# Kernel tuning notes

Measured on AMD Instinct MI355X. Metric: run time of the kernel, lower is better.

## Reference

```python
import jax, jax.numpy as jnp
import numpy as np

N, E = 50000, 800000
S, V, RBF_DIM = 128, 16, 16
RBF_DMAX = 20.0
MSG_NORM = 10.0
EPS = 1e-8
DVH_M = V + 1            # message GVP: dim_vectors_in = V + 1 (edge direction appended), dim_h = max(17,16) = 17
FIN_M = S + RBF_DIM      # message GVP scalar input = node scalars + rbf(dist)
DVH_U = 2 * V            # update GVP: dim_vectors_in = 2V (node + aggregated), dim_h = 32
FIN_U = 2 * S


def _rbf(D):
    # [E] -> [E, RBF_DIM], matches torch _rbf with D_min=0, D_max=20, D_count=16
    D_mu = jnp.linspace(0.0, RBF_DMAX, RBF_DIM)
    D_sigma = RBF_DMAX / RBF_DIM
    return jnp.exp(-(((D[:, None] - D_mu[None, :]) / D_sigma) ** 2))


def _gvp(s, v, Wh, Wu, Wf, bf, Wg, bg):
    # s: [n, F_in], v: [n, V_in, 3]; faithful to GVP.forward with sigmoid vector gating
    Vh = jnp.einsum('nvc,vh->nhc', v, Wh)          # [n, H, 3]
    Vu = jnp.einsum('nhc,ho->noc', Vh, Wu)         # [n, V_out, 3]
    sh = jnp.sqrt(jnp.clip(jnp.sum(Vh * Vh, -1), EPS))  # _norm_no_nan
    feats_out = jax.nn.silu(jnp.concatenate([s, sh], -1) @ Wf + bf)
    gate = jax.nn.sigmoid(feats_out @ Wg + bg)[..., None]
    return feats_out, gate * Vu


def _gvp_layernorm(s, v, gamma, beta):
    mu = jnp.mean(s, -1, keepdims=True)
    var = jnp.mean((s - mu) ** 2, -1, keepdims=True)
    s_out = (s - mu) / jnp.sqrt(var + 1e-5) * gamma + beta
    vn = jnp.clip(jnp.sum(v * v, -1, keepdims=True), EPS)        # [N, V, 1]
    vn = jnp.sqrt(jnp.mean(vn, -2, keepdims=True) + 1e-5) + 1e-5  # [N, 1, 1]
    return s_out, v / vn


def setup_inputs() -> dict:
    key = jax.random.key(0)
    ks = jax.random.split(key, 14)
    rn = lambda k, shp, sc: (jax.random.normal(k, shp, dtype=jnp.float32) * sc)
    inp = {
        's': rn(ks[0], (N, S), 1.0),
        'v': rn(ks[1], (N, V, 3), 1.0),
        'x': rn(ks[2], (N, 3), 5.0),
        # message GVP params
        'Wh_m': rn(ks[3], (DVH_M, DVH_M), 1.0 / np.sqrt(DVH_M)),
        'Wu_m': rn(ks[4], (DVH_M, V), 1.0 / np.sqrt(DVH_M)),
        'Wf_m': rn(ks[5], (DVH_M + FIN_M, S), 1.0 / np.sqrt(DVH_M + FIN_M)),
        'bf_m': jnp.zeros((S,), jnp.float32),
        'Wg_m': rn(ks[6], (S, V), 1.0 / np.sqrt(S)),
        'bg_m': jnp.zeros((V,), jnp.float32),
        # update GVP params
        'Wh_u': rn(ks[7], (DVH_U, DVH_U), 1.0 / np.sqrt(DVH_U)),
        'Wu_u': rn(ks[8], (DVH_U, V), 1.0 / np.sqrt(DVH_U)),
        'Wf_u': rn(ks[9], (DVH_U + FIN_U, S), 1.0 / np.sqrt(DVH_U + FIN_U)),
        'bf_u': jnp.zeros((S,), jnp.float32),
        'Wg_u': rn(ks[10], (S, V), 1.0 / np.sqrt(S)),
        'bg_u': jnp.zeros((V,), jnp.float32),
        # layernorm
        'ln_g': jnp.ones((S,), jnp.float32),
        'ln_b': jnp.zeros((S,), jnp.float32),
        'edge_index': jax.random.randint(ks[11], (2, E), 0, N),
    }
    return inp


def reference(s, v, x, Wh_m, Wu_m, Wf_m, bf_m, Wg_m, bg_m,
              Wh_u, Wu_u, Wf_u, bf_u, Wg_u, bg_u, ln_g, ln_b, edge_index):
    src, dst = edge_index[0], edge_index[1]
    # gather + geometric edge features
    dx = x[dst] - x[src]                                   # [E, 3]
    dist = jnp.sqrt(jnp.clip(jnp.sum(dx * dx, -1), EPS))    # [E]
    unit = dx / dist[:, None]
    v_in = jnp.concatenate([v[src], unit[:, None, :]], 1)   # [E, V+1, 3]
    s_in = jnp.concatenate([s[src], _rbf(dist)], -1)        # [E, S+RBF]
    # message GVP
    ms, mv = _gvp(s_in, v_in, Wh_m, Wu_m, Wf_m, bf_m, Wg_m, bg_m)
    # scatter-reduce + message norm
    agg_s = jax.ops.segment_sum(ms, dst, num_segments=N) / MSG_NORM   # [N, S]
    agg_v = jax.ops.segment_sum(mv, dst, num_segments=N) / MSG_NORM   # [N, V, 3]
    # update GVP on concatenated node + aggregated messages
    us, uv = _gvp(jnp.concatenate([s, agg_s], -1), jnp.concatenate([v, agg_v], 1),
                  Wh_u, Wu_u, Wf_u, bf_u, Wg_u, bg_u)
    # residual + GVPLayerNorm
    return _gvp_layernorm(s + us, v + uv, ln_g, ln_b)
```

## Files before the change

### kernel.cpp

```cpp
#include <hip/hip_runtime.h>
#include <hip/hip_bf16.h>
#include <math.h>

#define N_NODES 50000
#define E_EDGES 800000
#define S_DIM 128
#define V_DIM 16
#define HM 17
#define KM 161
#define HU 32
#define KU 288

#define EB 32
#define LDA 164
#define NB 32
#define LDA2 292

__device__ __forceinline__ float bf2f(unsigned short u) {
    union { unsigned int i; float f; } w; w.i = ((unsigned int)u) << 16; return w.f;
}
__device__ __forceinline__ unsigned short f2bf(float f) {
    union { float f; unsigned int i; } w; w.f = f;
    unsigned int x = w.i;
    x += 0x7fff + ((x >> 16) & 1);
    return (unsigned short)(x >> 16);
}
__device__ __forceinline__ float silu_f(float x) { return x / (1.f + __expf(-x)); }
__device__ __forceinline__ float sigm_f(float x) { return 1.f / (1.f + __expf(-x)); }
__device__ __forceinline__ float ldf(const void* p, int i, int m) {
    if (m) return ((const float*)p)[i];
    return bf2f(((const unsigned short*)p)[i]);
}

__global__ void detect_kernel(const unsigned short* __restrict__ s_us,
                              int* __restrict__ flag) {
    int t = threadIdx.x;
    int huge = 0;
    for (int k = 0; k < 16; ++k) {
        unsigned short u = s_us[2 * (t + 64 * k)];
        int e = (u >> 7) & 0xFF;
        if (e > 140) huge = 1;
    }
    if (huge) atomicOr(flag, 1);
}

__global__ __launch_bounds__(256, 4) void edge_kernel(
    const void* sP, const void* vP, const void* xP,
    const void* WhP, const void* WuP, const void* WfP,
    const void* bfP, const void* WgP, const void* bgP,
    const int* __restrict__ ei,
    const int* __restrict__ flagp,
    float* __restrict__ agg_s,
    float* __restrict__ agg_v)
{
    __shared__ float A[EB * LDA];
    __shared__ float Bs[2048];
    __shared__ float WhWu[HM * 16];
    __shared__ float gates[EB * 16];
    __shared__ int srcb[EB], dstb[EB];

    const int t = threadIdx.x;
    const int e0 = blockIdx.x * EB;
    const int m = flagp[0];

    if (t < EB) {
        srcb[t] = ei[e0 + t];
        dstb[t] = ei[E_EDGES + e0 + t];
    }
    if (m) {
        const float* Wh = (const float*)WhP;
        const float* Wu = (const float*)WuP;
        for (int i = t; i < HM * HM; i += 256) gates[i] = Wh[i];
        for (int i = t; i < HM * 16; i += 256) Bs[1664 + i] = Wu[i];
    } else {
        const unsigned short* Wh = (const unsigned short*)WhP;
        const unsigned short* Wu = (const unsigned short*)WuP;
        for (int i = t; i < HM * HM; i += 256) gates[i] = bf2f(Wh[i]);
        for (int i = t; i < HM * 16; i += 256) Bs[1664 + i] = bf2f(Wu[i]);
    }
    __syncthreads();

    for (int idx = t; idx < HM * 16; idx += 256) {
        int vv = idx / 16, o = idx % 16;
        float acc = 0.f;
        for (int h = 0; h < HM; ++h)
            acc += gates[vv * HM + h] * Bs[1664 + h * 16 + o];
        WhWu[idx] = acc;
    }
    {
        int tj = t & 31, te = t >> 5;
        if (m) {
            const float* sF = (const float*)sP;
            for (int r = 0; r < 4; ++r) {
                int e = te + 8 * r;
                float4 u = *(const float4*)(sF + (size_t)srcb[e] * S_DIM + tj * 4);
                float* a = &A[e * LDA + tj * 4];
                a[0] = u.x; a[1] = u.y; a[2] = u.z; a[3] = u.w;
            }
        } else {
            const unsigned short* sU = (const unsigned short*)sP;
            for (int r = 0; r < 4; ++r) {
                int e = te + 8 * r;
                ushort4 u = *(const ushort4*)(sU + (size_t)srcb[e] * S_DIM + tj * 4);
                float* a = &A[e * LDA + tj * 4];
                a[0] = bf2f(u.x); a[1] = bf2f(u.y); a[2] = bf2f(u.z); a[3] = bf2f(u.w);
            }
        }
    }
    if (t < 128) {
        int e = t >> 2, q = t & 3;
        int src = srcb[e];
        float* vin = &Bs[e * 52 + q * 12];
        if (m) {
            const float* vp = (const float*)vP + (size_t)src * 48 + q * 12;
            for (int i = 0; i < 3; ++i) {
                float4 u = *(const float4*)(vp + i * 4);
                vin[i * 4 + 0] = u.x; vin[i * 4 + 1] = u.y;
                vin[i * 4 + 2] = u.z; vin[i * 4 + 3] = u.w;
            }
        } else {
            const unsigned short* vp = (const unsigned short*)vP + (size_t)src * 48 + q * 12;
            for (int i = 0; i < 3; ++i) {
                ushort4 u = *(const ushort4*)(vp + i * 4);
                vin[i * 4 + 0] = bf2f(u.x); vin[i * 4 + 1] = bf2f(u.y);
                vin[i * 4 + 2] = bf2f(u.z); vin[i * 4 + 3] = bf2f(u.w);
            }
        }
        if (q == 0) {
            int dst = dstb[e];
            float dxc[3]; float d2 = 0.f;
            for (int c = 0; c < 3; ++c) {
                float xs = ldf(xP, src * 3 + c, m);
                float xd = ldf(xP, dst * 3 + c, m);
                dxc[c] = xd - xs; d2 += dxc[c] * dxc[c];
            }
            float dist = sqrtf(fmaxf(d2, 1e-8f));
            float inv = 1.f / dist;
            for (int c = 0; c < 3; ++c) Bs[e * 52 + 48 + c] = dxc[c] * inv;
            for (int k = 0; k < 16; ++k) {
                float mu = (20.f / 15.f) * (float)k;
                float z = (dist - mu) * (1.f / 1.25f);
                A[e * LDA + 128 + k] = __expf(-z * z);
            }
        }
    }
    __syncthreads();

    for (int idx = t; idx < EB * HM; idx += 256) {
        int e = idx / HM, h = idx % HM;
        const float* vin = &Bs[e * 52];
        float vh0 = 0.f, vh1 = 0.f, vh2 = 0.f;
        for (int vv = 0; vv < HM; ++vv) {
            float w = gates[vv * HM + h];
            vh0 += vin[vv * 3 + 0] * w;
            vh1 += vin[vv * 3 + 1] * w;
            vh2 += vin[vv * 3 + 2] * w;
        }
        A[e * LDA + 144 + h] = sqrtf(fmaxf(vh0 * vh0 + vh1 * vh1 + vh2 * vh2, 1e-8f));
    }
    float vureg[6];
    for (int r = 0; r < 6; ++r) {
        int idx = t + 256 * r;
        int e = idx / 48, oc = idx % 48, o = oc / 3, c = oc % 3;
        const float* vin = &Bs[e * 52];
        float acc = 0.f;
        for (int vv = 0; vv < HM; ++vv)
            acc += vin[vv * 3 + c] * WhWu[vv * 16 + o];
        vureg[r] = acc;
    }
    __syncthreads();

    const int tj = t & 15, te = t >> 4;
    const int eb = te * 2;
    float acc[2][8];
    #pragma unroll
    for (int i = 0; i < 2; ++i)
        #pragma unroll
        for (int j = 0; j < 8; ++j) acc[i][j] = 0.f;

    for (int kk = 0; kk < KM; kk += 16) {
        int kmax = min(16, KM - kk);
        if (m) {
            const float* WfF = (const float*)WfP;
            for (int idx = t; idx < kmax * 32; idx += 256) {
                int kt = idx >> 5, col4 = (idx & 31) * 4;
                float4 u = *(const float4*)(WfF + (size_t)(kk + kt) * 128 + col4);
                float* b = &Bs[kt * 128 + col4];
                b[0] = u.x; b[1] = u.y; b[2] = u.z; b[3] = u.w;
            }
        } else {
            const unsigned short* WfU = (const unsigned short*)WfP;
            for (int idx = t; idx < kmax * 32; idx += 256) {
                int kt = idx >> 5, col4 = (idx & 31) * 4;
                ushort4 u = *(const ushort4*)(WfU + (size_t)(kk + kt) * 128 + col4);
                float* b = &Bs[kt * 128 + col4];
                b[0] = bf2f(u.x); b[1] = bf2f(u.y); b[2] = bf2f(u.z); b[3] = bf2f(u.w);
            }
        }
        __syncthreads();
        for (int kt = 0; kt < kmax; ++kt) {
            float a0 = A[(eb + 0) * LDA + kk + kt];
            float a1 = A[(eb + 1) * LDA + kk + kt];
            const float* brow = &Bs[kt * 128 + tj];
            #pragma unroll
            for (int jj = 0; jj < 8; ++jj) {
                float b = brow[16 * jj];
                acc[0][jj] += a0 * b; acc[1][jj] += a1 * b;
            }
        }
        __syncthreads();
    }
    float breg[8];
    #pragma unroll
    for (int jj = 0; jj < 8; ++jj) breg[jj] = ldf(bfP, tj + 16 * jj, m);
    #pragma unroll
    for (int i = 0; i < 2; ++i) {
        int e = eb + i;
        float* aout = &A[e * LDA];
        float* gp = &agg_s[(size_t)dstb[e] * S_DIM];
        #pragma unroll
        for (int jj = 0; jj < 8; ++jj) {
            int col = tj + 16 * jj;
            float f = silu_f(acc[i][jj] + breg[jj]);
            aout[col] = f;
            atomicAdd(&gp[col], f);
        }
    }
    __syncthreads();
    if (m) {
        const float* Wg = (const float*)WgP;
        for (int i = t; i < 2048; i += 256) Bs[i] = Wg[i];
    } else {
        const unsigned short* Wg = (const unsigned short*)WgP;
        for (int i = t; i < 2048; i += 256) Bs[i] = bf2f(Wg[i]);
    }
    __syncthreads();
    for (int r = 0; r < 2; ++r) {
        int idx = t + 256 * r;
        int e = idx / 16, o = idx % 16;
        const float* fe = &A[e * LDA];
        float g = ldf(bgP, o, m);
        for (int j = 0; j < S_DIM; ++j)
            g += fe[j] * Bs[j * 16 + o];
        gates[idx] = sigm_f(g);
    }
    __syncthreads();
    for (int r = 0; r < 6; ++r) {
        int idx = t + 256 * r;
        int e = idx / 48, oc = idx % 48, o = oc / 3;
        float mvv = vureg[r] * gates[e * 16 + o];
        atomicAdd(&agg_v[(size_t)dstb[e] * 48 + oc], mvv);
    }
}

__global__ __launch_bounds__(256) void node_kernel(
    const void* sP, const void* vP,
    const void* WhP, const void* WuP, const void* WfP,
    const void* bfP, const void* WgP, const void* bgP,
    const void* lngP, const void* lnbP,
    const int* __restrict__ flagp,
    const float* __restrict__ agg_s,
    const float* __restrict__ agg_v,
    void* outP)
{
    __shared__ float A2[NB * LDA2];
    __shared__ float Bs2[4096];
    __shared__ float WhWu2[HU * 16];
    __shared__ float gates2[NB * 16];
    __shared__ float WhS[HU * HU];
    __shared__ float mu_s[NB], rstd_s[NB], vn_s[NB];

    const int t = threadIdx.x;
    const int n0 = blockIdx.x * NB;
    const int m = flagp[0];

    if (m) {
        const float* Wh = (const float*)WhP;
        const float* Wu = (const float*)WuP;
        for (int i = t; i < HU * HU; i += 256) WhS[i] = Wh[i];
        for (int i = t; i < HU * 16; i += 256) gates2[i] = Wu[i];
    } else {
        const unsigned short* Wh = (const unsigned short*)WhP;
        const unsigned short* Wu = (const unsigned short*)WuP;
        for (int i = t; i < HU * HU; i += 256) WhS[i] = bf2f(Wh[i]);
        for (int i = t; i < HU * 16; i += 256) gates2[i] = bf2f(Wu[i]);
    }
    if (m) {
        const float* sF = (const float*)sP;
        for (int idx = t; idx < NB * 32; idx += 256) {
            int ni = idx >> 5, col4 = (idx & 31) * 4;
            int n = n0 + ni;
            float* a = &A2[ni * LDA2 + col4];
            if (n < N_NODES) {
                float4 u = *(const float4*)(sF + (size_t)n * 128 + col4);
                a[0] = u.x; a[1] = u.y; a[2] = u.z; a[3] = u.w;
            } else { a[0] = a[1] = a[2] = a[3] = 0.f; }
        }
    } else {
        const unsigned short* sU = (const unsigned short*)sP;
        for (int idx = t; idx < NB * 32; idx += 256) {
            int ni = idx >> 5, col4 = (idx & 31) * 4;
            int n = n0 + ni;
            float* a = &A2[ni * LDA2 + col4];
            if (n < N_NODES) {
                ushort4 u = *(const ushort4*)(sU + (size_t)n * 128 + col4);
                a[0] = bf2f(u.x); a[1] = bf2f(u.y); a[2] = bf2f(u.z); a[3] = bf2f(u.w);
            } else { a[0] = a[1] = a[2] = a[3] = 0.f; }
        }
    }
    for (int idx = t; idx < NB * 32; idx += 256) {
        int ni = idx >> 5, col4 = (idx & 31) * 4;
        int n = n0 + ni;
        float* a = &A2[ni * LDA2 + 128 + col4];
        if (n < N_NODES) {
            float4 u = *(const float4*)(agg_s + (size_t)n * 128 + col4);
            a[0] = u.x * 0.1f; a[1] = u.y * 0.1f; a[2] = u.z * 0.1f; a[3] = u.w * 0.1f;
        } else { a[0] = a[1] = a[2] = a[3] = 0.f; }
    }
    for (int idx = t; idx < NB * 96; idx += 256) {
        int ni = idx / 96, vc = idx % 96;
        int n = n0 + ni;
        float val = 0.f;
        if (n < N_NODES)
            val = (vc < 48) ? ldf(vP, n * 48 + vc, m)
                            : agg_v[(size_t)n * 48 + (vc - 48)] * 0.1f;
        Bs2[ni * 100 + vc] = val;
    }
    __syncthreads();
    for (int idx = t; idx < HU * 16; idx += 256) {
        int vv = idx / 16, o = idx % 16;
        float acc = 0.f;
        for (int h = 0; h < HU; ++h)
            acc += WhS[vv * HU + h] * gates2[h * 16 + o];
        WhWu2[idx] = acc;
    }
    for (int idx = t; idx < NB * HU; idx += 256) {
        int ni = idx / HU, h = idx % HU;
        const float* vc = &Bs2[ni * 100];
        float vh0 = 0.f, vh1 = 0.f, vh2 = 0.f;
        for (int vv = 0; vv < HU; ++vv) {
            float w = WhS[vv * HU + h];
            vh0 += vc[vv * 3 + 0] * w; vh1 += vc[vv * 3 + 1] * w; vh2 += vc[vv * 3 + 2] * w;
        }
        A2[ni * LDA2 + 256 + h] = sqrtf(fmaxf(vh0 * vh0 + vh1 * vh1 + vh2 * vh2, 1e-8f));
    }
    __syncthreads();
    float vureg[6];
    for (int r = 0; r < 6; ++r) {
        int idx = t + 256 * r;
        int ni = idx / 48, oc = idx % 48, o = oc / 3, c = oc % 3;
        const float* vc = &Bs2[ni * 100];
        float acc = 0.f;
        for (int vv = 0; vv < HU; ++vv)
            acc += vc[vv * 3 + c] * WhWu2[vv * 16 + o];
        vureg[r] = acc;
    }
    __syncthreads();

    const int tj = t & 15, tn = t >> 4;
    const int nb = tn * 2;
    float acc[2][8];
    #pragma unroll
    for (int i = 0; i < 2; ++i)
        #pragma unroll
        for (int j = 0; j < 8; ++j) acc[i][j] = 0.f;

    for (int kk = 0; kk < KU; kk += 32) {
        if (m) {
            const float* WfF = (const float*)WfP;
            for (int idx = t; idx < 32 * 32; idx += 256) {
                int kt = idx >> 5, col4 = (idx & 31) * 4;
                float4 u = *(const float4*)(WfF + (size_t)(kk + kt) * 128 + col4);
                float* b = &Bs2[kt * 128 + col4];
                b[0] = u.x; b[1] = u.y; b[2] = u.z; b[3] = u.w;
            }
        } else {
            const unsigned short* WfU = (const unsigned short*)WfP;
            for (int idx = t; idx < 32 * 32; idx += 256) {
                int kt = idx >> 5, col4 = (idx & 31) * 4;
                ushort4 u = *(const ushort4*)(WfU + (size_t)(kk + kt) * 128 + col4);
                float* b = &Bs2[kt * 128 + col4];
                b[0] = bf2f(u.x); b[1] = bf2f(u.y); b[2] = bf2f(u.z); b[3] = bf2f(u.w);
            }
        }
        __syncthreads();
        for (int kt = 0; kt < 32; ++kt) {
            float a0 = A2[(nb + 0) * LDA2 + kk + kt];
            float a1 = A2[(nb + 1) * LDA2 + kk + kt];
            const float* brow = &Bs2[kt * 128 + tj];
            #pragma unroll
            for (int jj = 0; jj < 8; ++jj) {
                float b = brow[16 * jj];
                acc[0][jj] += a0 * b; acc[1][jj] += a1 * b;
            }
        }
        __syncthreads();
    }
    float breg[8];
    #pragma unroll
    for (int jj = 0; jj < 8; ++jj) breg[jj] = ldf(bfP, tj + 16 * jj, m);
    #pragma unroll
    for (int i = 0; i < 2; ++i) {
        float* aout = &A2[(nb + i) * LDA2 + 128];
        #pragma unroll
        for (int jj = 0; jj < 8; ++jj)
            aout[tj + 16 * jj] = silu_f(acc[i][jj] + breg[jj]);
    }
    __syncthreads();
    if (m) {
        const float* Wg = (const float*)WgP;
        for (int i = t; i < 2048; i += 256) Bs2[i] = Wg[i];
    } else {
        const unsigned short* Wg = (const unsigned short*)WgP;
        for (int i = t; i < 2048; i += 256) Bs2[i] = bf2f(Wg[i]);
    }
    __syncthreads();
    for (int r = 0; r < 2; ++r) {
        int idx = t + 256 * r;
        int ni = idx / 16, o = idx % 16;
        const float* fe = &A2[ni * LDA2 + 128];
        float g = ldf(bgP, o, m);
        for (int j = 0; j < 128; ++j)
            g += fe[j] * Bs2[j * 16 + o];
        gates2[idx] = sigm_f(g);
    }
    __syncthreads();
    for (int r = 0; r < 6; ++r) {
        int idx = t + 256 * r;
        int ni = idx / 48, oc = idx % 48, o = oc / 3;
        int n = n0 + ni;
        float vres = 0.f;
        if (n < N_NODES)
            vres = ldf(vP, n * 48 + oc, m) + vureg[r] * gates2[ni * 16 + o];
        Bs2[ni * 48 + oc] = vres;
    }
    __syncthreads();
    if (t < NB) {
        const float* arow = &A2[t * LDA2];
        float sum = 0.f, sumsq = 0.f;
        for (int j = 0; j < 128; ++j) {
            float xr = arow[j] + arow[128 + j];
            sum += xr; sumsq += xr * xr;
        }
        float mu = sum * (1.f / 128.f);
        float var = sumsq * (1.f / 128.f) - mu * mu;
        mu_s[t] = mu;
        rstd_s[t] = rsqrtf(fmaxf(var, 0.f) + 1e-5f);
        const float* vr = &Bs2[t * 48];
        float accv = 0.f;
        for (int o = 0; o < 16; ++o) {
            float mm = vr[o*3]*vr[o*3] + vr[o*3+1]*vr[o*3+1] + vr[o*3+2]*vr[o*3+2];
            accv += fmaxf(mm, 1e-8f);
        }
        vn_s[t] = sqrtf(accv * (1.f / 16.f) + 1e-5f) + 1e-5f;
    }
    __syncthreads();
    float* outF = (float*)outP;
    unsigned short* outU = (unsigned short*)outP;
    for (int idx = t; idx < NB * 128; idx += 256) {
        int ni = idx >> 7, j = idx & 127;
        int n = n0 + ni;
        if (n < N_NODES) {
            float xr = A2[ni * LDA2 + j] + A2[ni * LDA2 + 128 + j];
            float o = (xr - mu_s[ni]) * rstd_s[ni] * ldf(lngP, j, m) + ldf(lnbP, j, m);
            if (m) outF[(size_t)n * 128 + j] = o;
            else   outU[(size_t)n * 128 + j] = f2bf(o);
        }
    }
    for (int idx = t; idx < NB * 48; idx += 256) {
        int ni = idx / 48, oc = idx % 48;
        int n = n0 + ni;
        if (n < N_NODES) {
            float o = Bs2[ni * 48 + oc] / vn_s[ni];
            if (m) outF[(size_t)N_NODES * 128 + (size_t)n * 48 + oc] = o;
            else   outU[(size_t)N_NODES * 128 + (size_t)n * 48 + oc] = f2bf(o);
        }
    }
}

extern "C" void kernel_launch(void* const* d_in, const int* in_sizes, int n_in,
                              void* d_out, int out_size, void* d_ws, size_t ws_size,
                              hipStream_t stream) {
    const int* ei = (const int*)d_in[17];

    int* flag = (int*)d_ws;
    float* agg_s = (float*)((char*)d_ws + 64);
    float* agg_v = agg_s + (size_t)N_NODES * 128;
    hipMemsetAsync(d_ws, 0, 64 + (size_t)N_NODES * (128 + 48) * sizeof(float), stream);

    detect_kernel<<<1, 64, 0, stream>>>((const unsigned short*)d_in[0], flag);

    edge_kernel<<<E_EDGES / EB, 256, 0, stream>>>(
        d_in[0], d_in[1], d_in[2], d_in[3], d_in[4], d_in[5],
        d_in[6], d_in[7], d_in[8], ei, flag, agg_s, agg_v);
    node_kernel<<<(N_NODES + NB - 1) / NB, 256, 0, stream>>>(
        d_in[0], d_in[1], d_in[9], d_in[10], d_in[11], d_in[12],
        d_in[13], d_in[14], d_in[15], d_in[16], flag,
        agg_s, agg_v, d_out);
}
```

Before: 2.401 ms.

## Sort edges by destination and pre-reduce runs before atomic scatter

Adds a histogram, scan and counting-sort pass that reorders edges by destination node, so each edge block holds runs of edges sharing a destination. The edge kernel then sums scalar and vector messages along each run in shared memory and issues one atomic per run per column, instead of one atomic per edge per column. The GEMM inner loops in both kernels also switch to contiguous per-thread columns with float4 shared-memory loads. The sort adds three extra launches, including a single-block serial scan, and sorting scatters the source gathers. Atomic ordering within the scatter is nondeterministic, which changes float summation order.

Measured after the change: 2.726 ms. +13.6%, slower.

```diff
diff --git a/kernel.cpp b/kernel.cpp
--- a/kernel.cpp
+++ b/kernel.cpp
@@ -44,11 +44,55 @@
     if (huge) atomicOr(flag, 1);
 }
 
+__global__ __launch_bounds__(256) void hist_kernel(const int* __restrict__ ei,
+                                                   int* __restrict__ deg) {
+    int e = blockIdx.x * 256 + threadIdx.x;
+    if (e < E_EDGES) atomicAdd(&deg[ei[E_EDGES + e]], 1);
+}
+
+__global__ __launch_bounds__(1024) void scan_kernel(const int* __restrict__ deg,
+                                                    int* __restrict__ cursor) {
+    __shared__ int part[1024];
+    const int t = threadIdx.x;
+    const int CH = 49;
+    int base = t * CH;
+    int s = 0;
+    for (int i = 0; i < CH; ++i) {
+        int idx = base + i;
+        if (idx < N_NODES) s += deg[idx];
+    }
+    part[t] = s;
+    __syncthreads();
+    if (t == 0) {
+        int run = 0;
+        for (int i = 0; i < 1024; ++i) { int tmp = part[i]; part[i] = run; run += tmp; }
+    }
+    __syncthreads();
+    int run = part[t];
+    for (int i = 0; i < CH; ++i) {
+        int idx = base + i;
+        if (idx < N_NODES) { cursor[idx] = run; run += deg[idx]; }
+    }
+}
+
+__global__ __launch_bounds__(256) void scatter_kernel(const int* __restrict__ ei,
+                                                      int* __restrict__ cursor,
+                                                      int* __restrict__ ssrc,
+                                                      int* __restrict__ sdst) {
+    int e = blockIdx.x * 256 + threadIdx.x;
+    if (e >= E_EDGES) return;
+    int src = ei[e], dst = ei[E_EDGES + e];
+    int pos = atomicAdd(&cursor[dst], 1);
+    ssrc[pos] = src;
+    sdst[pos] = dst;
+}
+
 __global__ __launch_bounds__(256, 4) void edge_kernel(
     const void* sP, const void* vP, const void* xP,
     const void* WhP, const void* WuP, const void* WfP,
     const void* bfP, const void* WgP, const void* bgP,
-    const int* __restrict__ ei,
+    const int* __restrict__ ssrc,
+    const int* __restrict__ sdst,
     const int* __restrict__ flagp,
     float* __restrict__ agg_s,
     float* __restrict__ agg_v)
@@ -64,8 +108,8 @@
     const int m = flagp[0];
 
     if (t < EB) {
-        srcb[t] = ei[e0 + t];
-        dstb[t] = ei[E_EDGES + e0 + t];
+        srcb[t] = ssrc[e0 + t];
+        dstb[t] = sdst[e0 + t];
     }
     if (m) {
         const float* Wh = (const float*)WhP;
@@ -172,6 +216,7 @@
 
     const int tj = t & 15, te = t >> 4;
     const int eb = te * 2;
+    const int j0 = tj * 8;
     float acc[2][8];
     #pragma unroll
     for (int i = 0; i < 2; ++i)
@@ -198,33 +243,46 @@
             }
         }
         __syncthreads();
-        for (int kt = 0; kt < kmax; ++kt) {
+        int kt = 0;
+        for (; kt + 3 < kmax; kt += 4) {
+            float4 a0 = *(const float4*)&A[(eb + 0) * LDA + kk + kt];
+            float4 a1 = *(const float4*)&A[(eb + 1) * LDA + kk + kt];
+            const float a0v[4] = {a0.x, a0.y, a0.z, a0.w};
+            const float a1v[4] = {a1.x, a1.y, a1.z, a1.w};
+            #pragma unroll
+            for (int q = 0; q < 4; ++q) {
+                const float* brow = &Bs[(kt + q) * 128 + j0];
+                float4 bl = *(const float4*)brow;
+                float4 bh = *(const float4*)(brow + 4);
+                const float bv[8] = {bl.x, bl.y, bl.z, bl.w, bh.x, bh.y, bh.z, bh.w};
+                #pragma unroll
+                for (int j = 0; j < 8; ++j) {
+                    acc[0][j] += a0v[q] * bv[j];
+                    acc[1][j] += a1v[q] * bv[j];
+                }
+            }
+        }
+        for (; kt < kmax; ++kt) {
             float a0 = A[(eb + 0) * LDA + kk + kt];
             float a1 = A[(eb + 1) * LDA + kk + kt];
-            const float* brow = &Bs[kt * 128 + tj];
+            const float* brow = &Bs[kt * 128 + j0];
             #pragma unroll
-            for (int jj = 0; jj < 8; ++jj) {
-                float b = brow[16 * jj];
-                acc[0][jj] += a0 * b; acc[1][jj] += a1 * b;
+            for (int j = 0; j < 8; ++j) {
+                float b = brow[j];
+                acc[0][j] += a0 * b; acc[1][j] += a1 * b;
             }
         }
         __syncthreads();
     }
     float breg[8];
     #pragma unroll
-    for (int jj = 0; jj < 8; ++jj) breg[jj] = ldf(bfP, tj + 16 * jj, m);
+    for (int j = 0; j < 8; ++j) breg[j] = ldf(bfP, j0 + j, m);
     #pragma unroll
     for (int i = 0; i < 2; ++i) {
-        int e = eb + i;
-        float* aout = &A[e * LDA];
-        float* gp = &agg_s[(size_t)dstb[e] * S_DIM];
+        float* aout = &A[(eb + i) * LDA + j0];
         #pragma unroll
-        for (int jj = 0; jj < 8; ++jj) {
-            int col = tj + 16 * jj;
-            float f = silu_f(acc[i][jj] + breg[jj]);
-            aout[col] = f;
-            atomicAdd(&gp[col], f);
-        }
+        for (int j = 0; j < 8; ++j)
+            aout[j] = silu_f(acc[i][j] + breg[j]);
     }
     __syncthreads();
     if (m) {
@@ -248,8 +306,22 @@
     for (int r = 0; r < 6; ++r) {
         int idx = t + 256 * r;
         int e = idx / 48, oc = idx % 48, o = oc / 3;
-        float mvv = vureg[r] * gates[e * 16 + o];
-        atomicAdd(&agg_v[(size_t)dstb[e] * 48 + oc], mvv);
+        Bs[e * 48 + oc] = vureg[r] * gates[e * 16 + o];
+    }
+    __syncthreads();
+    if (t < 176) {
+        int c = t;
+        float racc = 0.f;
+        for (int e = 0; e < EB; ++e) {
+            racc += (c < 128) ? A[e * LDA + c] : Bs[e * 48 + (c - 128)];
+            bool flush = (e == EB - 1) || (dstb[e + 1] != dstb[e]);
+            if (flush) {
+                int d = dstb[e];
+                if (c < 128) atomicAdd(&agg_s[(size_t)d * 128 + c], racc);
+                else         atomicAdd(&agg_v[(size_t)d * 48 + (c - 128)], racc);
+                racc = 0.f;
+            }
+        }
     }
 }
 
@@ -359,6 +431,7 @@
 
     const int tj = t & 15, tn = t >> 4;
     const int nb = tn * 2;
+    const int j0 = tj * 8;
     float acc[2][8];
     #pragma unroll
     for (int i = 0; i < 2; ++i)
@@ -384,27 +457,35 @@
             }
         }
         __syncthreads();
-        for (int kt = 0; kt < 32; ++kt) {
-            float a0 = A2[(nb + 0) * LDA2 + kk + kt];
-            float a1 = A2[(nb + 1) * LDA2 + kk + kt];
-            const float* brow = &Bs2[kt * 128 + tj];
+        for (int kt = 0; kt < 32; kt += 4) {
+            float4 a0 = *(const float4*)&A2[(nb + 0) * LDA2 + kk + kt];
+            float4 a1 = *(const float4*)&A2[(nb + 1) * LDA2 + kk + kt];
+            const float a0v[4] = {a0.x, a0.y, a0.z, a0.w};
+            const float a1v[4] = {a1.x, a1.y, a1.z, a1.w};
             #pragma unroll
-            for (int jj = 0; jj < 8; ++jj) {
-                float b = brow[16 * jj];
-                acc[0][jj] += a0 * b; acc[1][jj] += a1 * b;
+            for (int q = 0; q < 4; ++q) {
+                const float* brow = &Bs2[(kt + q) * 128 + j0];
+                float4 bl = *(const float4*)brow;
+                float4 bh = *(const float4*)(brow + 4);
+                const float bv[8] = {bl.x, bl.y, bl.z, bl.w, bh.x, bh.y, bh.z, bh.w};
+                #pragma unroll
+                for (int j = 0; j < 8; ++j) {
+                    acc[0][j] += a0v[q] * bv[j];
+                    acc[1][j] += a1v[q] * bv[j];
+                }
             }
         }
         __syncthreads();
     }
     float breg[8];
     #pragma unroll
-    for (int jj = 0; jj < 8; ++jj) breg[jj] = ldf(bfP, tj + 16 * jj, m);
+    for (int j = 0; j < 8; ++j) breg[j] = ldf(bfP, j0 + j, m);
     #pragma unroll
     for (int i = 0; i < 2; ++i) {
-        float* aout = &A2[(nb + i) * LDA2 + 128];
+        float* aout = &A2[(nb + i) * LDA2 + 128 + j0];
         #pragma unroll
-        for (int jj = 0; jj < 8; ++jj)
-            aout[tj + 16 * jj] = silu_f(acc[i][jj] + breg[jj]);
+        for (int j = 0; j < 8; ++j)
+            aout[j] = silu_f(acc[i][j] + breg[j]);
     }
     __syncthreads();
     if (m) {
@@ -483,16 +564,26 @@
                               hipStream_t stream) {
     const int* ei = (const int*)d_in[17];
 
-    int* flag = (int*)d_ws;
-    float* agg_s = (float*)((char*)d_ws + 64);
-    float* agg_v = agg_s + (size_t)N_NODES * 128;
-    hipMemsetAsync(d_ws, 0, 64 + (size_t)N_NODES * (128 + 48) * sizeof(float), stream);
+    char* base = (char*)d_ws;
+    int*   flag   = (int*)base;
+    float* agg_s  = (float*)(base + 64);
+    float* agg_v  = agg_s + (size_t)N_NODES * 128;
+    int*   deg    = (int*)(base + 64 + (size_t)N_NODES * (128 + 48) * 4);
+    int*   cursor = deg + N_NODES;
+    int*   ssrc   = cursor + N_NODES;
+    int*   sdst   = ssrc + E_EDGES;
+
+    size_t zero_bytes = 64 + (size_t)N_NODES * (128 + 48) * 4 + (size_t)N_NODES * 4;
+    hipMemsetAsync(d_ws, 0, zero_bytes, stream);
 
     detect_kernel<<<1, 64, 0, stream>>>((const unsigned short*)d_in[0], flag);
+    hist_kernel<<<(E_EDGES + 255) / 256, 256, 0, stream>>>(ei, deg);
+    scan_kernel<<<1, 1024, 0, stream>>>(deg, cursor);
+    scatter_kernel<<<(E_EDGES + 255) / 256, 256, 0, stream>>>(ei, cursor, ssrc, sdst);
 
     edge_kernel<<<E_EDGES / EB, 256, 0, stream>>>(
         d_in[0], d_in[1], d_in[2], d_in[3], d_in[4], d_in[5],
-        d_in[6], d_in[7], d_in[8], ei, flag, agg_s, agg_v);
+        d_in[6], d_in[7], d_in[8], ssrc, sdst, flag, agg_s, agg_v);
     node_kernel<<<(N_NODES + NB - 1) / NB, 256, 0, stream>>>(
         d_in[0], d_in[1], d_in[9], d_in[10], d_in[11], d_in[12],
         d_in[13], d_in[14], d_in[15], d_in[16], flag,
```

## Sort edges by destination (CSR) and reduce messages in shared memory

Applied to the files above, without the earlier changes.

Builds a destination-sorted edge list using histogram, single-block scan and atomic scatter kernels. Each edge block now owns 8 destination nodes, loops over their incoming edges in tiles of 32, segment-reduces message scalars and vectors in shared memory, and writes agg_s/agg_v once with plain stores, replacing per-element global float atomics. In exchange it adds three preprocessing kernels, a serial scan, load imbalance from varying degree per block, partially filled edge tiles, and a serial per-column reduction loop.

After: 3.865 ms. 61.0% more time.

```diff
diff --git a/kernel.cpp b/kernel.cpp
--- a/kernel.cpp
+++ b/kernel.cpp
@@ -12,6 +12,7 @@
 #define KU 288
 
 #define EB 32
+#define DPB 8
 #define LDA 164
 #define NB 32
 #define LDA2 292
@@ -44,11 +45,57 @@
     if (huge) atomicOr(flag, 1);
 }
 
+__global__ __launch_bounds__(256) void hist_kernel(const int* __restrict__ ei,
+                                                   int* __restrict__ deg) {
+    int e = blockIdx.x * 256 + threadIdx.x;
+    if (e < E_EDGES) atomicAdd(&deg[ei[E_EDGES + e]], 1);
+}
+
+__global__ __launch_bounds__(1024) void scan_kernel(const int* __restrict__ deg,
+                                                    int* __restrict__ cursor,
+                                                    int* __restrict__ row_ptr) {
+    __shared__ int part[1024];
+    const int t = threadIdx.x;
+    const int CH = 49;
+    int base = t * CH;
+    int s = 0;
+    for (int i = 0; i < CH; ++i) {
+        int idx = base + i;
+        if (idx < N_NODES) s += deg[idx];
+    }
+    part[t] = s;
+    __syncthreads();
+    if (t == 0) {
+        int run = 0;
+        for (int i = 0; i < 1024; ++i) { int tmp = part[i]; part[i] = run; run += tmp; }
+    }
+    __syncthreads();
+    int run = part[t];
+    for (int i = 0; i < CH; ++i) {
+        int idx = base + i;
+        if (idx < N_NODES) { cursor[idx] = run; row_ptr[idx] = run; run += deg[idx]; }
+    }
+}
+
+__global__ __launch_bounds__(256) void scatter_kernel(const int* __restrict__ ei,
+                                                      int* __restrict__ cursor,
+                                                      int* __restrict__ ssrc,
+                                                      int* __restrict__ sdst) {
+    int e = blockIdx.x * 256 + threadIdx.x;
+    if (e >= E_EDGES) return;
+    int src = ei[e], dst = ei[E_EDGES + e];
+    int pos = atomicAdd(&cursor[dst], 1);
+    ssrc[pos] = src;
+    sdst[pos] = dst;
+}
+
 __global__ __launch_bounds__(256, 4) void edge_kernel(
     const void* sP, const void* vP, const void* xP,
     const void* WhP, const void* WuP, const void* WfP,
     const void* bfP, const void* WgP, const void* bgP,
-    const int* __restrict__ ei,
+    const int* __restrict__ row_ptr,
+    const int* __restrict__ ssrc,
+    const int* __restrict__ sdst,
     const int* __restrict__ flagp,
     float* __restrict__ agg_s,
     float* __restrict__ agg_v)
@@ -56,200 +103,225 @@
     __shared__ float A[EB * LDA];
     __shared__ float Bs[2048];
     __shared__ float WhWu[HM * 16];
+    __shared__ float WhS[HM * HM + 3];
     __shared__ float gates[EB * 16];
+    __shared__ float agg[DPB * 176];
     __shared__ int srcb[EB], dstb[EB];
 
     const int t = threadIdx.x;
-    const int e0 = blockIdx.x * EB;
     const int m = flagp[0];
-
-    if (t < EB) {
-        srcb[t] = ei[e0 + t];
-        dstb[t] = ei[E_EDGES + e0 + t];
-    }
+    const int d0 = blockIdx.x * DPB;
+    const int e_beg = row_ptr[d0];
+    const int e_end = (d0 + DPB >= N_NODES) ? E_EDGES : row_ptr[d0 + DPB];
+
+    for (int i = t; i < DPB * 176; i += 256) agg[i] = 0.f;
     if (m) {
         const float* Wh = (const float*)WhP;
         const float* Wu = (const float*)WuP;
-        for (int i = t; i < HM * HM; i += 256) gates[i] = Wh[i];
+        for (int i = t; i < HM * HM; i += 256) WhS[i] = Wh[i];
         for (int i = t; i < HM * 16; i += 256) Bs[1664 + i] = Wu[i];
     } else {
         const unsigned short* Wh = (const unsigned short*)WhP;
         const unsigned short* Wu = (const unsigned short*)WuP;
-        for (int i = t; i < HM * HM; i += 256) gates[i] = bf2f(Wh[i]);
+        for (int i = t; i < HM * HM; i += 256) WhS[i] = bf2f(Wh[i]);
         for (int i = t; i < HM * 16; i += 256) Bs[1664 + i] = bf2f(Wu[i]);
     }
     __syncthreads();
-
     for (int idx = t; idx < HM * 16; idx += 256) {
         int vv = idx / 16, o = idx % 16;
         float acc = 0.f;
         for (int h = 0; h < HM; ++h)
-            acc += gates[vv * HM + h] * Bs[1664 + h * 16 + o];
+            acc += WhS[vv * HM + h] * Bs[1664 + h * 16 + o];
         WhWu[idx] = acc;
-    }
-    {
-        int tj = t & 31, te = t >> 5;
-        if (m) {
-            const float* sF = (const float*)sP;
-            for (int r = 0; r < 4; ++r) {
-                int e = te + 8 * r;
-                float4 u = *(const float4*)(sF + (size_t)srcb[e] * S_DIM + tj * 4);
-                float* a = &A[e * LDA + tj * 4];
-                a[0] = u.x; a[1] = u.y; a[2] = u.z; a[3] = u.w;
-            }
-        } else {
-            const unsigned short* sU = (const unsigned short*)sP;
-            for (int r = 0; r < 4; ++r) {
-                int e = te + 8 * r;
-                ushort4 u = *(const ushort4*)(sU + (size_t)srcb[e] * S_DIM + tj * 4);
-                float* a = &A[e * LDA + tj * 4];
-                a[0] = bf2f(u.x); a[1] = bf2f(u.y); a[2] = bf2f(u.z); a[3] = bf2f(u.w);
-            }
-        }
-    }
-    if (t < 128) {
-        int e = t >> 2, q = t & 3;
-        int src = srcb[e];
-        float* vin = &Bs[e * 52 + q * 12];
-        if (m) {
-            const float* vp = (const float*)vP + (size_t)src * 48 + q * 12;
-            for (int i = 0; i < 3; ++i) {
-                float4 u = *(const float4*)(vp + i * 4);
-                vin[i * 4 + 0] = u.x; vin[i * 4 + 1] = u.y;
-                vin[i * 4 + 2] = u.z; vin[i * 4 + 3] = u.w;
-            }
-        } else {
-            const unsigned short* vp = (const unsigned short*)vP + (size_t)src * 48 + q * 12;
-            for (int i = 0; i < 3; ++i) {
-                ushort4 u = *(const ushort4*)(vp + i * 4);
-                vin[i * 4 + 0] = bf2f(u.x); vin[i * 4 + 1] = bf2f(u.y);
-                vin[i * 4 + 2] = bf2f(u.z); vin[i * 4 + 3] = bf2f(u.w);
-            }
-        }
-        if (q == 0) {
-            int dst = dstb[e];
-            float dxc[3]; float d2 = 0.f;
-            for (int c = 0; c < 3; ++c) {
-                float xs = ldf(xP, src * 3 + c, m);
-                float xd = ldf(xP, dst * 3 + c, m);
-                dxc[c] = xd - xs; d2 += dxc[c] * dxc[c];
-            }
-            float dist = sqrtf(fmaxf(d2, 1e-8f));
-            float inv = 1.f / dist;
-            for (int c = 0; c < 3; ++c) Bs[e * 52 + 48 + c] = dxc[c] * inv;
-            for (int k = 0; k < 16; ++k) {
-                float mu = (20.f / 15.f) * (float)k;
-                float z = (dist - mu) * (1.f / 1.25f);
-                A[e * LDA + 128 + k] = __expf(-z * z);
-            }
-        }
-    }
-    __syncthreads();
-
-    for (int idx = t; idx < EB * HM; idx += 256) {
-        int e = idx / HM, h = idx % HM;
-        const float* vin = &Bs[e * 52];
-        float vh0 = 0.f, vh1 = 0.f, vh2 = 0.f;
-        for (int vv = 0; vv < HM; ++vv) {
-            float w = gates[vv * HM + h];
-            vh0 += vin[vv * 3 + 0] * w;
-            vh1 += vin[vv * 3 + 1] * w;
-            vh2 += vin[vv * 3 + 2] * w;
-        }
-        A[e * LDA + 144 + h] = sqrtf(fmaxf(vh0 * vh0 + vh1 * vh1 + vh2 * vh2, 1e-8f));
-    }
-    float vureg[6];
-    for (int r = 0; r < 6; ++r) {
-        int idx = t + 256 * r;
-        int e = idx / 48, oc = idx % 48, o = oc / 3, c = oc % 3;
-        const float* vin = &Bs[e * 52];
-        float acc = 0.f;
-        for (int vv = 0; vv < HM; ++vv)
-            acc += vin[vv * 3 + c] * WhWu[vv * 16 + o];
-        vureg[r] = acc;
     }
     __syncthreads();
 
     const int tj = t & 15, te = t >> 4;
     const int eb = te * 2;
-    float acc[2][8];
-    #pragma unroll
-    for (int i = 0; i < 2; ++i)
+
+    for (int et = e_beg; et < e_end; et += EB) {
+        const int cnt = min(EB, e_end - et);
+        if (t < EB) {
+            srcb[t] = (t < cnt) ? ssrc[et + t] : 0;
+            dstb[t] = (t < cnt) ? (sdst[et + t] - d0) : 0;
+        }
+        __syncthreads();
+        {
+            int cj = t & 31, ce = t >> 5;
+            if (m) {
+                const float* sF = (const float*)sP;
+                for (int r = 0; r < 4; ++r) {
+                    int e = ce + 8 * r;
+                    float4 u = *(const float4*)(sF + (size_t)srcb[e] * S_DIM + cj * 4);
+                    float* a = &A[e * LDA + cj * 4];
+                    a[0] = u.x; a[1] = u.y; a[2] = u.z; a[3] = u.w;
+                }
+            } else {
+                const unsigned short* sU = (const unsigned short*)sP;
+                for (int r = 0; r < 4; ++r) {
+                    int e = ce + 8 * r;
+                    ushort4 u = *(const ushort4*)(sU + (size_t)srcb[e] * S_DIM + cj * 4);
+                    float* a = &A[e * LDA + cj * 4];
+                    a[0] = bf2f(u.x); a[1] = bf2f(u.y); a[2] = bf2f(u.z); a[3] = bf2f(u.w);
+                }
+            }
+        }
+        if (t < 128) {
+            int e = t >> 2, q = t & 3;
+            int src = srcb[e];
+            float* vin = &Bs[e * 52 + q * 12];
+            if (m) {
+                const float* vp = (const float*)vP + (size_t)src * 48 + q * 12;
+                for (int i = 0; i < 3; ++i) {
+                    float4 u = *(const float4*)(vp + i * 4);
+                    vin[i * 4 + 0] = u.x; vin[i * 4 + 1] = u.y;
+                    vin[i * 4 + 2] = u.z; vin[i * 4 + 3] = u.w;
+                }
+            } else {
+                const unsigned short* vp = (const unsigned short*)vP + (size_t)src * 48 + q * 12;
+                for (int i = 0; i < 3; ++i) {
+                    ushort4 u = *(const ushort4*)(vp + i * 4);
+                    vin[i * 4 + 0] = bf2f(u.x); vin[i * 4 + 1] = bf2f(u.y);
+                    vin[i * 4 + 2] = bf2f(u.z); vin[i * 4 + 3] = bf2f(u.w);
+                }
+            }
+            if (q == 0) {
+                int dst = d0 + dstb[e];
+                float dxc[3]; float d2 = 0.f;
+                for (int c = 0; c < 3; ++c) {
+                    float xs = ldf(xP, src * 3 + c, m);
+                    float xd = ldf(xP, dst * 3 + c, m);
+                    dxc[c] = xd - xs; d2 += dxc[c] * dxc[c];
+                }
+                float dist = sqrtf(fmaxf(d2, 1e-8f));
+                float inv = 1.f / dist;
+                for (int c = 0; c < 3; ++c) Bs[e * 52 + 48 + c] = dxc[c] * inv;
+                for (int k = 0; k < 16; ++k) {
+                    float mu = (20.f / 15.f) * (float)k;
+                    float z = (dist - mu) * (1.f / 1.25f);
+                    A[e * LDA + 128 + k] = __expf(-z * z);
+                }
+            }
+        }
+        __syncthreads();
+        for (int idx = t; idx < EB * HM; idx += 256) {
+            int e = idx / HM, h = idx % HM;
+            const float* vin = &Bs[e * 52];
+            float vh0 = 0.f, vh1 = 0.f, vh2 = 0.f;
+            for (int vv = 0; vv < HM; ++vv) {
+                float w = WhS[vv * HM + h];
+                vh0 += vin[vv * 3 + 0] * w;
+                vh1 += vin[vv * 3 + 1] * w;
+                vh2 += vin[vv * 3 + 2] * w;
+            }
+            A[e * LDA + 144 + h] = sqrtf(fmaxf(vh0 * vh0 + vh1 * vh1 + vh2 * vh2, 1e-8f));
+        }
+        float vureg[6];
+        for (int r = 0; r < 6; ++r) {
+            int idx = t + 256 * r;
+            int e = idx / 48, oc = idx % 48, o = oc / 3, c = oc % 3;
+            const float* vin = &Bs[e * 52];
+            float acc = 0.f;
+            for (int vv = 0; vv < HM; ++vv)
+                acc += vin[vv * 3 + c] * WhWu[vv * 16 + o];
+            vureg[r] = acc;
+        }
+        __syncthreads();
+
+        float acc[2][8];
         #pragma unroll
-        for (int j = 0; j < 8; ++j) acc[i][j] = 0.f;
-
-    for (int kk = 0; kk < KM; kk += 16) {
-        int kmax = min(16, KM - kk);
-        if (m) {
-            const float* WfF = (const float*)WfP;
-            for (int idx = t; idx < kmax * 32; idx += 256) {
-                int kt = idx >> 5, col4 = (idx & 31) * 4;
-                float4 u = *(const float4*)(WfF + (size_t)(kk + kt) * 128 + col4);
-                float* b = &Bs[kt * 128 + col4];
-                b[0] = u.x; b[1] = u.y; b[2] = u.z; b[3] = u.w;
-            }
-        } else {
-            const unsigned short* WfU = (const unsigned short*)WfP;
-            for (int idx = t; idx < kmax * 32; idx += 256) {
-                int kt = idx >> 5, col4 = (idx & 31) * 4;
-                ushort4 u = *(const ushort4*)(WfU + (size_t)(kk + kt) * 128 + col4);
-                float* b = &Bs[kt * 128 + col4];
-                b[0] = bf2f(u.x); b[1] = bf2f(u.y); b[2] = bf2f(u.z); b[3] = bf2f(u.w);
-            }
-        }
-        __syncthreads();
-        for (int kt = 0; kt < kmax; ++kt) {
-            float a0 = A[(eb + 0) * LDA + kk + kt];
-            float a1 = A[(eb + 1) * LDA + kk + kt];
-            const float* brow = &Bs[kt * 128 + tj];
+        for (int i = 0; i < 2; ++i)
+            #pragma unroll
+            for (int j = 0; j < 8; ++j) acc[i][j] = 0.f;
+
+        for (int kk = 0; kk < KM; kk += 16) {
+            int kmax = min(16, KM - kk);
+            if (m) {
+                const float* WfF = (const float*)WfP;
+                for (int idx = t; idx < kmax * 32; idx += 256) {
+                    int kt = idx >> 5, col4 = (idx & 31) * 4;
+                    float4 u = *(const float4*)(WfF + (size_t)(kk + kt) * 128 + col4);
+                    float* b = &Bs[kt * 128 + col4];
+                    b[0] = u.x; b[1] = u.y; b[2] = u.z; b[3] = u.w;
+                }
+            } else {
+                const unsigned short* WfU = (const unsigned short*)WfP;
+                for (int idx = t; idx < kmax * 32; idx += 256) {
+                    int kt = idx >> 5, col4 = (idx & 31) * 4;
+                    ushort4 u = *(const ushort4*)(WfU + (size_t)(kk + kt) * 128 + col4);
+                    float* b = &Bs[kt * 128 + col4];
+                    b[0] = bf2f(u.x); b[1] = bf2f(u.y); b[2] = bf2f(u.z); b[3] = bf2f(u.w);
+                }
+            }
+            __syncthreads();
+            for (int kt = 0; kt < kmax; ++kt) {
+                float a0 = A[(eb + 0) * LDA + kk + kt];
+                float a1 = A[(eb + 1) * LDA + kk + kt];
+                const float* brow = &Bs[kt * 128 + tj];
+                #pragma unroll
+                for (int jj = 0; jj < 8; ++jj) {
+                    float b = brow[16 * jj];
+                    acc[0][jj] += a0 * b; acc[1][jj] += a1 * b;
+                }
+            }
+            __syncthreads();
+        }
+        float breg[8];
+        #pragma unroll
+        for (int jj = 0; jj < 8; ++jj) breg[jj] = ldf(bfP, tj + 16 * jj, m);
+        #pragma unroll
+        for (int i = 0; i < 2; ++i) {
+            float* aout = &A[(eb + i) * LDA];
             #pragma unroll
             for (int jj = 0; jj < 8; ++jj) {
-                float b = brow[16 * jj];
-                acc[0][jj] += a0 * b; acc[1][jj] += a1 * b;
-            }
-        }
-        __syncthreads();
-    }
-    float breg[8];
-    #pragma unroll
-    for (int jj = 0; jj < 8; ++jj) breg[jj] = ldf(bfP, tj + 16 * jj, m);
-    #pragma unroll
-    for (int i = 0; i < 2; ++i) {
-        int e = eb + i;
-        float* aout = &A[e * LDA];
-        float* gp = &agg_s[(size_t)dstb[e] * S_DIM];
-        #pragma unroll
-        for (int jj = 0; jj < 8; ++jj) {
-            int col = tj + 16 * jj;
-            float f = silu_f(acc[i][jj] + breg[jj]);
-            aout[col] = f;
-            atomicAdd(&gp[col], f);
-        }
-    }
-    __syncthreads();
-    if (m) {
-        const float* Wg = (const float*)WgP;
-        for (int i = t; i < 2048; i += 256) Bs[i] = Wg[i];
-    } else {
-        const unsigned short* Wg = (const unsigned short*)WgP;
-        for (int i = t; i < 2048; i += 256) Bs[i] = bf2f(Wg[i]);
-    }
-    __syncthreads();
-    for (int r = 0; r < 2; ++r) {
-        int idx = t + 256 * r;
-        int e = idx / 16, o = idx % 16;
-        const float* fe = &A[e * LDA];
-        float g = ldf(bgP, o, m);
-        for (int j = 0; j < S_DIM; ++j)
-            g += fe[j] * Bs[j * 16 + o];
-        gates[idx] = sigm_f(g);
-    }
-    __syncthreads();
-    for (int r = 0; r < 6; ++r) {
-        int idx = t + 256 * r;
-        int e = idx / 48, oc = idx % 48, o = oc / 3;
-        float mvv = vureg[r] * gates[e * 16 + o];
-        atomicAdd(&agg_v[(size_t)dstb[e] * 48 + oc], mvv);
+                int col = tj + 16 * jj;
+                aout[col] = silu_f(acc[i][jj] + breg[jj]);
+            }
+        }
+        __syncthreads();
+        if (m) {
+            const float* Wg = (const float*)WgP;
+            for (int i = t; i < 2048; i += 256) Bs[i] = Wg[i];
+        } else {
+            const unsigned short* Wg = (const unsigned short*)WgP;
+            for (int i = t; i < 2048; i += 256) Bs[i] = bf2f(Wg[i]);
+        }
+        __syncthreads();
+        for (int r = 0; r < 2; ++r) {
+            int idx = t + 256 * r;
+            int e = idx / 16, o = idx % 16;
+            const float* fe = &A[e * LDA];
+            float g = ldf(bgP, o, m);
+            for (int j = 0; j < S_DIM; ++j)
+                g += fe[j] * Bs[j * 16 + o];
+            gates[idx] = sigm_f(g);
+        }
+        __syncthreads();
+        for (int r = 0; r < 6; ++r) {
+            int idx = t + 256 * r;
+            int e = idx / 48, oc = idx % 48, o = oc / 3;
+            Bs[e * 48 + oc] = vureg[r] * gates[e * 16 + o];
+        }
+        __syncthreads();
+        if (t < 176) {
+            int c = t;
+            float racc = 0.f;
+            for (int e = 0; e < cnt; ++e) {
+                racc += (c < 128) ? A[e * LDA + c] : Bs[e * 48 + (c - 128)];
+                bool flush = (e == cnt - 1) || (dstb[e + 1] != dstb[e]);
+                if (flush) {
+                    agg[dstb[e] * 176 + c] += racc;
+                    racc = 0.f;
+                }
+            }
+        }
+        __syncthreads();
+    }
+    for (int idx = t; idx < DPB * 176; idx += 256) {
+        int d = idx / 176, c = idx % 176;
+        int n = d0 + d;
+        if (c < 128) agg_s[(size_t)n * 128 + c] = agg[idx];
+        else         agg_v[(size_t)n * 48 + (c - 128)] = agg[idx];
     }
 }
 
@@ -403,8 +475,10 @@
     for (int i = 0; i < 2; ++i) {
         float* aout = &A2[(nb + i) * LDA2 + 128];
         #pragma unroll
-        for (int jj = 0; jj < 8; ++jj)
-            aout[tj + 16 * jj] = silu_f(acc[i][jj] + breg[jj]);
+        for (int jj = 0; jj < 8; ++jj) {
+            int col = tj + 16 * jj;
+            aout[col] = silu_f(acc[i][jj] + breg[jj]);
+        }
     }
     __syncthreads();
     if (m) {
@@ -483,18 +557,28 @@
                               hipStream_t stream) {
     const int* ei = (const int*)d_in[17];
 
-    int* flag = (int*)d_ws;
-    float* agg_s = (float*)((char*)d_ws + 64);
-    float* agg_v = agg_s + (size_t)N_NODES * 128;
-    hipMemsetAsync(d_ws, 0, 64 + (size_t)N_NODES * (128 + 48) * sizeof(float), stream);
+    char* base = (char*)d_ws;
+    int*   flag    = (int*)base;
+    int*   deg     = (int*)(base + 64);
+    int*   cursor  = deg + N_NODES;
+    int*   row_ptr = cursor + N_NODES;
+    int*   ssrc    = row_ptr + N_NODES;
+    int*   sdst    = ssrc + E_EDGES;
+    float* agg_s   = (float*)(sdst + E_EDGES);
+    float* agg_v   = agg_s + (size_t)N_NODES * 128;
+
+    hipMemsetAsync(d_ws, 0, 64 + (size_t)N_NODES * 4, stream);
 
     detect_kernel<<<1, 64, 0, stream>>>((const unsigned short*)d_in[0], flag);
-
-    edge_kernel<<<E_EDGES / EB, 256, 0, stream>>>(
+    hist_kernel<<<(E_EDGES + 255) / 256, 256, 0, stream>>>(ei, deg);
+    scan_kernel<<<1, 1024, 0, stream>>>(deg, cursor, row_ptr);
+    scatter_kernel<<<(E_EDGES + 255) / 256, 256, 0, stream>>>(ei, cursor, ssrc, sdst);
+
+    edge_kernel<<<N_NODES / DPB, 256, 0, stream>>>(
         d_in[0], d_in[1], d_in[2], d_in[3], d_in[4], d_in[5],
-        d_in[6], d_in[7], d_in[8], ei, flag, agg_s, agg_v);
+        d_in[6], d_in[7], d_in[8], row_ptr, ssrc, sdst, flag, agg_s, agg_v);
     node_kernel<<<(N_NODES + NB - 1) / NB, 256, 0, stream>>>(
         d_in[0], d_in[1], d_in[9], d_in[10], d_in[11], d_in[12],
         d_in[13], d_in[14], d_in[15], d_in[16], flag,
-        agg_s, agg_v, d_out);
-}
+        agg_s, agg_v, (void*)d_out);
+}
```
